# Kernel optimization log

Measured on AMD Instinct MI355X. Metric: run time of the kernel, lower is better.

Reference implementation:

```python
import jax, jax.numpy as jnp
import numpy as np
import math

S, B, L, D = 4096, 2048, 256, 128  # substructure pool, batch, max substructs/drug, hidden


def setup_inputs() -> dict:
    key = jax.random.key(0)
    ks = jax.random.split(key, 6)
    sub_feat = jax.random.normal(ks[0], (S, D), dtype=jnp.float32)
    sub_index = jax.random.randint(ks[1], (B, L), 0, S)
    # ragged lengths -> padded prefix mask (1.0 = valid substructure)
    lengths = jax.random.randint(ks[2], (B,), 8, L + 1)
    mask = (jnp.arange(L)[None, :] < lengths[:, None]).astype(jnp.float32)
    scale = 1.0 / math.sqrt(D)
    Wq = jax.random.normal(ks[3], (D, D), dtype=jnp.float32) * scale
    Wk = jax.random.normal(ks[4], (D, D), dtype=jnp.float32) * scale
    bq = jnp.zeros((D,), dtype=jnp.float32)
    bk = jnp.zeros((D,), dtype=jnp.float32)
    return {"sub_feat": sub_feat, "mask": mask, "Wq": Wq, "bq": bq,
            "Wk": Wk, "bk": bk, "sub_index": sub_index}


def reference(sub_feat, mask, Wq, bq, Wk, bk, sub_index):
    # per-drug gather of substructure ('expert') features: [B, L, D]
    gathered = sub_feat[sub_index]
    # single-head Q/K projections (V is computed but unused in the original)
    q = gathered @ Wq + bq  # [B, L, D]
    k = gathered @ Wk + bk  # [B, L, D]
    inv_sqrt_d = 1.0 / math.sqrt(D)
    # additive mask: (1 - m) * -10000 broadcast over query dim
    add_mask = (1.0 - mask)[:, None, :] * -10000.0  # [B, 1, L]
    scores = jnp.einsum('bid,bjd->bij', q, k) * inv_sqrt_d + add_mask  # [B, L, L]
    probs = jax.nn.softmax(scores, axis=-1)
    # O[:, 0, 0, :] in the original: head 0, query position 0
    score = probs[:, 0, :]  # [B, L]
    # drug_feat[i] = score[i] @ sub_feat[sub_index[i]]
    drug_embeddings = jnp.einsum('bl,bld->bd', score, gathered)  # [B, D]
    return drug_embeddings
```

## Files before the change

### kernel.cpp

```cpp
#include <hip/hip_runtime.h>

#define DIM 128
#define LEN 256
#define INV_SQRT_D 0.08838834764831845f
#define LOG2E 1.4426950408889634f
#define SCALE_L2 (INV_SQRT_D * LOG2E)

#define WS_MT   0
#define WS_C    (DIM * DIM)
#define WS_W2   (DIM * DIM + DIM)
#define WS_BQBK (DIM * DIM + 2 * DIM)
#define WS_BF   (DIM * DIM + 2 * DIM + 8)

__device__ __forceinline__ float bl(unsigned u) { return __uint_as_float(u << 16); }
__device__ __forceinline__ float bh(unsigned u) { return __uint_as_float(u & 0xffff0000u); }

__global__ __launch_bounds__(256) void prep_kernel(
    const float* __restrict__ sub_feat,
    const float* __restrict__ Wq, const float* __restrict__ bq,
    const float* __restrict__ Wk, const float* __restrict__ bk,
    float* __restrict__ ws, ushort* __restrict__ bfb, int n4)
{
    const int t   = threadIdx.x;
    const int bid = blockIdx.x;

    if (bid < DIM) {
        if (t < DIM) {
            __shared__ float wqj[DIM];
            wqj[t] = Wq[bid * DIM + t];
            __syncthreads();
            const float4* row = reinterpret_cast<const float4*>(Wk + t * DIM);
            float acc = 0.f;
            #pragma unroll 8
            for (int i = 0; i < DIM / 4; ++i) {
                float4 u = row[i];
                acc = fmaf(u.x, wqj[4*i+0], acc);
                acc = fmaf(u.y, wqj[4*i+1], acc);
                acc = fmaf(u.z, wqj[4*i+2], acc);
                acc = fmaf(u.w, wqj[4*i+3], acc);
            }
            ws[WS_MT + bid * DIM + t] = acc;
        } else {
            __syncthreads();
        }
    } else if (bid == DIM) {
        if (t < DIM) {
            __shared__ float bqs[DIM], bks[DIM], red[DIM];
            bqs[t] = bq[t]; bks[t] = bk[t];
            __syncthreads();
            const float4* rk = reinterpret_cast<const float4*>(Wk + t * DIM);
            const float4* rq = reinterpret_cast<const float4*>(Wq + t * DIM);
            float accC = 0.f, accW = 0.f;
            #pragma unroll 8
            for (int i = 0; i < DIM / 4; ++i) {
                float4 a  = rk[i];
                float4 b2 = rq[i];
                accC = fmaf(a.x,  bqs[4*i+0], accC);
                accC = fmaf(a.y,  bqs[4*i+1], accC);
                accC = fmaf(a.z,  bqs[4*i+2], accC);
                accC = fmaf(a.w,  bqs[4*i+3], accC);
                accW = fmaf(b2.x, bks[4*i+0], accW);
                accW = fmaf(b2.y, bks[4*i+1], accW);
                accW = fmaf(b2.z, bks[4*i+2], accW);
                accW = fmaf(b2.w, bks[4*i+3], accW);
            }
            ws[WS_C  + t] = accC;
            ws[WS_W2 + t] = accW;
            red[t] = bqs[t] * bks[t];
            __syncthreads();
            if (t == 0) {
                float s = 0.f;
                for (int i = 0; i < DIM; ++i) s += red[i];
                ws[WS_BQBK] = s;
            }
        } else {
            __syncthreads(); __syncthreads();
        }
    } else {
        const int i = (bid - DIM - 1) * 256 + t;
        if (i < n4) {
            const float4 u = reinterpret_cast<const float4*>(sub_feat)[i];
            ushort4 o;
            unsigned a;
            a = __float_as_uint(u.x); o.x = (ushort)((a + 0x7fffu + ((a >> 16) & 1u)) >> 16);
            a = __float_as_uint(u.y); o.y = (ushort)((a + 0x7fffu + ((a >> 16) & 1u)) >> 16);
            a = __float_as_uint(u.z); o.z = (ushort)((a + 0x7fffu + ((a >> 16) & 1u)) >> 16);
            a = __float_as_uint(u.w); o.w = (ushort)((a + 0x7fffu + ((a >> 16) & 1u)) >> 16);
            reinterpret_cast<ushort4*>(bfb)[i] = o;
        }
    }
}

__global__ __launch_bounds__(256, 8) void main_kernel(
    const float* __restrict__ sub_feat, const ushort* __restrict__ gfeat,
    const float* __restrict__ mask, const int* __restrict__ sub_index,
    const float* __restrict__ ws, float* __restrict__ out)
{
    const int t    = threadIdx.x;
    const int lane = t & 63;
    const int wv   = t >> 6;
    const int b    = blockIdx.x;
    const int g    = lane >> 4;
    const int m16  = lane & 15;

    __shared__ float2 ibw[LEN];
    __shared__ float  g0L[DIM];
    __shared__ float  vh [2][DIM];
    __shared__ float  vL [DIM];
    __shared__ float  OW [4][DIM];
    __shared__ float  Zw [4];
    __shared__ float  qbkL;

    {
        const int   ij = sub_index[(size_t)b * LEN + t];
        const float mk = mask[(size_t)b * LEN + t];
        ibw[t] = make_float2(__int_as_float(ij), (1.f - mk) * (-10000.f * LOG2E));
    }
    if (t < 64) {
        const int r0 = sub_index[(size_t)b * LEN];
        const float2 g0p = reinterpret_cast<const float2*>(sub_feat + (size_t)r0 * DIM)[t];
        g0L[2 * t]     = g0p.x;
        g0L[2 * t + 1] = g0p.y;
        const float* w2 = ws + WS_W2;
        float qp = g0p.x * w2[2 * t] + g0p.y * w2[2 * t + 1];
        #pragma unroll
        for (int o = 32; o > 0; o >>= 1) qp += __shfl_xor(qp, o);
        if (t == 0) qbkL = (qp + ws[WS_BQBK]) * SCALE_L2;
    }
    __syncthreads();

    {
        const int i  = t & (DIM - 1);
        const int hh = t >> 7;
        const float* Mrow = ws + WS_MT + hh * 64 * DIM;
        const float* gL   = g0L + hh * 64;
        float a = 0.f;
        #pragma unroll 8
        for (int j = 0; j < 64; ++j)
            a = fmaf(gL[j], Mrow[j * DIM + i], a);
        vh[hh][i] = a;
    }
    __syncthreads();
    if (t < DIM) {
        vL[t] = (vh[0][t] + vh[1][t] + ws[WS_C + t]) * SCALE_L2;
    }
    __syncthreads();

    const float4 va = reinterpret_cast<const float4*>(vL)[2 * m16];
    const float4 vb = reinterpret_cast<const float4*>(vL)[2 * m16 + 1];
    const float qterm = qbkL;

    float Zr = 0.f;
    float O0=0.f,O1=0.f,O2=0.f,O3=0.f,O4=0.f,O5=0.f,O6=0.f,O7=0.f;

    const int jbase = wv * 64;
    #pragma unroll 4
    for (int k = 0; k < 16; ++k) {
        const float2 ibp = ibw[jbase + 4 * k + g];
        const int   ij = __float_as_int(ibp.x);
        const float bj = ibp.y;
        const uint4 u = *reinterpret_cast<const uint4*>(gfeat + (size_t)ij * DIM + 8 * m16);
        const float f0 = bl(u.x), f1 = bh(u.x), f2 = bl(u.y), f3 = bh(u.y);
        const float f4 = bl(u.z), f5 = bh(u.z), f6 = bl(u.w), f7 = bh(u.w);
        float sd = f0*va.x + f1*va.y + f2*va.z + f3*va.w
                 + f4*vb.x + f5*vb.y + f6*vb.z + f7*vb.w;
        sd += __shfl_xor(sd, 1);
        sd += __shfl_xor(sd, 2);
        sd += __shfl_xor(sd, 4);
        sd += __shfl_xor(sd, 8);
        const float e = exp2f(sd + qterm + bj);
        Zr += e;
        O0 = fmaf(e, f0, O0); O1 = fmaf(e, f1, O1);
        O2 = fmaf(e, f2, O2); O3 = fmaf(e, f3, O3);
        O4 = fmaf(e, f4, O4); O5 = fmaf(e, f5, O5);
        O6 = fmaf(e, f6, O6); O7 = fmaf(e, f7, O7);
    }

    #pragma unroll
    for (int msk = 16; msk <= 32; msk <<= 1) {
        Zr += __shfl_xor(Zr, msk);
        O0 += __shfl_xor(O0, msk); O1 += __shfl_xor(O1, msk);
        O2 += __shfl_xor(O2, msk); O3 += __shfl_xor(O3, msk);
        O4 += __shfl_xor(O4, msk); O5 += __shfl_xor(O5, msk);
        O6 += __shfl_xor(O6, msk); O7 += __shfl_xor(O7, msk);
    }
    if (lane < 16) {
        reinterpret_cast<float4*>(&OW[wv][0])[2 * m16]     = make_float4(O0, O1, O2, O3);
        reinterpret_cast<float4*>(&OW[wv][0])[2 * m16 + 1] = make_float4(O4, O5, O6, O7);
    }
    if (lane == 0) Zw[wv] = Zr;
    __syncthreads();

    if (t < DIM) {
        const float Zt = Zw[0] + Zw[1] + Zw[2] + Zw[3];
        out[(size_t)b * DIM + t] =
            (OW[0][t] + OW[1][t] + OW[2][t] + OW[3][t]) / Zt;
    }
}

__global__ __launch_bounds__(256) void fused_fallback(
    const float* __restrict__ sub_feat, const float* __restrict__ mask,
    const int* __restrict__ sub_index, const float* __restrict__ ws,
    float* __restrict__ out)
{
    const int t    = threadIdx.x;
    const int lane = t & 63;
    const int wv   = t >> 6;
    const int b    = blockIdx.x;
    const int g    = lane >> 4;
    const int m16  = lane & 15;

    __shared__ float2 ibw[LEN];
    __shared__ float  g0L[DIM];
    __shared__ float  vh [2][DIM];
    __shared__ float  vL [DIM];
    __shared__ float  OW [4][DIM];
    __shared__ float  Zw [4];
    __shared__ float  qbkL;

    {
        const int   ij = sub_index[(size_t)b * LEN + t];
        const float mk = mask[(size_t)b * LEN + t];
        ibw[t] = make_float2(__int_as_float(ij), (1.f - mk) * (-10000.f * LOG2E));
    }
    if (t < 64) {
        const int r0 = sub_index[(size_t)b * LEN];
        const float2 g0p = reinterpret_cast<const float2*>(sub_feat + (size_t)r0 * DIM)[t];
        g0L[2 * t]     = g0p.x;
        g0L[2 * t + 1] = g0p.y;
        const float* w2 = ws + WS_W2;
        float qp = g0p.x * w2[2 * t] + g0p.y * w2[2 * t + 1];
        #pragma unroll
        for (int o = 32; o > 0; o >>= 1) qp += __shfl_xor(qp, o);
        if (t == 0) qbkL = (qp + ws[WS_BQBK]) * SCALE_L2;
    }
    __syncthreads();
    {
        const int i  = t & (DIM - 1);
        const int hh = t >> 7;
        const float* Mrow = ws + WS_MT + hh * 64 * DIM;
        const float* gL   = g0L + hh * 64;
        float a = 0.f;
        #pragma unroll 8
        for (int j = 0; j < 64; ++j)
            a = fmaf(gL[j], Mrow[j * DIM + i], a);
        vh[hh][i] = a;
    }
    __syncthreads();
    if (t < DIM) vL[t] = (vh[0][t] + vh[1][t] + ws[WS_C + t]) * SCALE_L2;
    __syncthreads();

    const float4 vAa = reinterpret_cast<const float4*>(vL)[2 * m16];
    const float4 vBb = reinterpret_cast<const float4*>(vL)[2 * m16 + 1];
    const float qterm = qbkL;

    float Zr = 0.f;
    float O0=0.f,O1=0.f,O2=0.f,O3=0.f,O4=0.f,O5=0.f,O6=0.f,O7=0.f;
    const int jbase = wv * 64;
    #pragma unroll 4
    for (int k = 0; k < 16; ++k) {
        const float2 ibp = ibw[jbase + 4 * k + g];
        const int   ij = __float_as_int(ibp.x);
        const float bj = ibp.y;
        const float* rp = sub_feat + (size_t)ij * DIM + 8 * m16;
        const float4 u0 = *reinterpret_cast<const float4*>(rp);
        const float4 u1 = *reinterpret_cast<const float4*>(rp + 4);
        float sd = u0.x*vAa.x + u0.y*vAa.y + u0.z*vAa.z + u0.w*vAa.w
                 + u1.x*vBb.x + u1.y*vBb.y + u1.z*vBb.z + u1.w*vBb.w;
        sd += __shfl_xor(sd, 1);
        sd += __shfl_xor(sd, 2);
        sd += __shfl_xor(sd, 4);
        sd += __shfl_xor(sd, 8);
        const float e = exp2f(sd + qterm + bj);
        Zr += e;
        O0 = fmaf(e, u0.x, O0); O1 = fmaf(e, u0.y, O1);
        O2 = fmaf(e, u0.z, O2); O3 = fmaf(e, u0.w, O3);
        O4 = fmaf(e, u1.x, O4); O5 = fmaf(e, u1.y, O5);
        O6 = fmaf(e, u1.z, O6); O7 = fmaf(e, u1.w, O7);
    }
    #pragma unroll
    for (int msk = 16; msk <= 32; msk <<= 1) {
        Zr += __shfl_xor(Zr, msk);
        O0 += __shfl_xor(O0, msk); O1 += __shfl_xor(O1, msk);
        O2 += __shfl_xor(O2, msk); O3 += __shfl_xor(O3, msk);
        O4 += __shfl_xor(O4, msk); O5 += __shfl_xor(O5, msk);
        O6 += __shfl_xor(O6, msk); O7 += __shfl_xor(O7, msk);
    }
    if (lane < 16) {
        reinterpret_cast<float4*>(&OW[wv][0])[2 * m16]     = make_float4(O0, O1, O2, O3);
        reinterpret_cast<float4*>(&OW[wv][0])[2 * m16 + 1] = make_float4(O4, O5, O6, O7);
    }
    if (lane == 0) Zw[wv] = Zr;
    __syncthreads();

    if (t < DIM) {
        const float Zt = Zw[0] + Zw[1] + Zw[2] + Zw[3];
        out[(size_t)b * DIM + t] =
            (OW[0][t] + OW[1][t] + OW[2][t] + OW[3][t]) / Zt;
    }
}

extern "C" void kernel_launch(void* const* d_in, const int* in_sizes, int n_in,
                              void* d_out, int out_size, void* d_ws, size_t ws_size,
                              hipStream_t stream) {
    const float* sub_feat  = (const float*)d_in[0];
    const float* mask      = (const float*)d_in[1];
    const float* Wq        = (const float*)d_in[2];
    const float* bq        = (const float*)d_in[3];
    const float* Wk        = (const float*)d_in[4];
    const float* bk        = (const float*)d_in[5];
    const int*   sub_index = (const int*)d_in[6];
    float* outp = (float*)d_out;
    float* ws   = (float*)d_ws;

    const int B  = in_sizes[6] / LEN;
    const int SD = in_sizes[0];
    const int n4 = SD / 4;

    const size_t needed = ((size_t)WS_BF + (size_t)(SD + 1) / 2) * sizeof(float);

    if (ws_size >= needed) {
        ushort* bfb = reinterpret_cast<ushort*>(ws + WS_BF);
        const int cvt_blocks = (n4 + 255) / 256;
        prep_kernel<<<dim3(DIM + 1 + cvt_blocks), dim3(256), 0, stream>>>(
            sub_feat, Wq, bq, Wk, bk, ws, bfb, n4);
        main_kernel<<<dim3(B), dim3(256), 0, stream>>>(
            sub_feat, bfb, mask, sub_index, ws, outp);
    } else {
        prep_kernel<<<dim3(DIM + 1), dim3(256), 0, stream>>>(
            sub_feat, Wq, bq, Wk, bk, ws, nullptr, 0);
        fused_fallback<<<dim3(B), dim3(256), 0, stream>>>(
            sub_feat, mask, sub_index, ws, outp);
    }
}
```

Before: 29.32 us.

## Fuse prep and main kernels into one cooperative launch with grid sync

Merges the weight-folding/bf16-conversion prep kernel and the per-drug attention kernel into a single cooperative kernel. Prep blocks do their prep work, every block stages its indices and mask, and a grid-wide sync separates the phases. The aim is to remove the second kernel launch and the gap between the two kernels. In exchange it adds a grid barrier and host-side device-property and occupancy queries on every call, and it only takes this path when all B blocks can be resident at once.

```diff
diff --git a/kernel.cpp b/kernel.cpp
--- a/kernel.cpp
+++ b/kernel.cpp
@@ -1,4 +1,7 @@
 #include <hip/hip_runtime.h>
+#include <hip/hip_cooperative_groups.h>
+
+namespace cg = cooperative_groups;
 
 #define DIM 128
 #define LEN 256
@@ -15,20 +18,27 @@
 __device__ __forceinline__ float bl(unsigned u) { return __uint_as_float(u << 16); }
 __device__ __forceinline__ float bh(unsigned u) { return __uint_as_float(u & 0xffff0000u); }
 
-__global__ __launch_bounds__(256) void prep_kernel(
+struct MainSmem {
+    float2 ibw[LEN];
+    float  g0L[DIM];
+    float  vh[2][DIM];
+    float  vL[DIM];
+    float  OW[4][DIM];
+    float  Zw[4];
+    float  qbkL;
+};
+
+__device__ __forceinline__ void prep_unit(int unit, int t,
     const float* __restrict__ sub_feat,
     const float* __restrict__ Wq, const float* __restrict__ bq,
     const float* __restrict__ Wk, const float* __restrict__ bk,
     float* __restrict__ ws, ushort* __restrict__ bfb, int n4)
 {
-    const int t   = threadIdx.x;
-    const int bid = blockIdx.x;
-
-    if (bid < DIM) {
+    if (unit < DIM) {
+        __shared__ float wqj[DIM];
+        if (t < DIM) wqj[t] = Wq[unit * DIM + t];
+        __syncthreads();
         if (t < DIM) {
-            __shared__ float wqj[DIM];
-            wqj[t] = Wq[bid * DIM + t];
-            __syncthreads();
             const float4* row = reinterpret_cast<const float4*>(Wk + t * DIM);
             float acc = 0.f;
             #pragma unroll 8
@@ -39,15 +49,13 @@
                 acc = fmaf(u.z, wqj[4*i+2], acc);
                 acc = fmaf(u.w, wqj[4*i+3], acc);
             }
-            ws[WS_MT + bid * DIM + t] = acc;
-        } else {
-            __syncthreads();
-        }
-    } else if (bid == DIM) {
+            ws[WS_MT + unit * DIM + t] = acc;
+        }
+    } else if (unit == DIM) {
+        __shared__ float bqs[DIM], bks[DIM], red[DIM];
+        if (t < DIM) { bqs[t] = bq[t]; bks[t] = bk[t]; }
+        __syncthreads();
         if (t < DIM) {
-            __shared__ float bqs[DIM], bks[DIM], red[DIM];
-            bqs[t] = bq[t]; bks[t] = bk[t];
-            __syncthreads();
             const float4* rk = reinterpret_cast<const float4*>(Wk + t * DIM);
             const float4* rq = reinterpret_cast<const float4*>(Wq + t * DIM);
             float accC = 0.f, accW = 0.f;
@@ -67,17 +75,15 @@
             ws[WS_C  + t] = accC;
             ws[WS_W2 + t] = accW;
             red[t] = bqs[t] * bks[t];
-            __syncthreads();
-            if (t == 0) {
-                float s = 0.f;
-                for (int i = 0; i < DIM; ++i) s += red[i];
-                ws[WS_BQBK] = s;
-            }
-        } else {
-            __syncthreads(); __syncthreads();
+        }
+        __syncthreads();
+        if (t == 0) {
+            float s = 0.f;
+            for (int i = 0; i < DIM; ++i) s += red[i];
+            ws[WS_BQBK] = s;
         }
     } else {
-        const int i = (bid - DIM - 1) * 256 + t;
+        const int i = (unit - DIM - 1) * 256 + t;
         if (i < n4) {
             const float4 u = reinterpret_cast<const float4*>(sub_feat)[i];
             ushort4 o;
@@ -91,64 +97,56 @@
     }
 }
 
-__global__ __launch_bounds__(256, 8) void main_kernel(
-    const float* __restrict__ sub_feat, const ushort* __restrict__ gfeat,
-    const float* __restrict__ mask, const int* __restrict__ sub_index,
-    const float* __restrict__ ws, float* __restrict__ out)
-{
-    const int t    = threadIdx.x;
-    const int lane = t & 63;
-    const int wv   = t >> 6;
-    const int b    = blockIdx.x;
-    const int g    = lane >> 4;
-    const int m16  = lane & 15;
-
-    __shared__ float2 ibw[LEN];
-    __shared__ float  g0L[DIM];
-    __shared__ float  vh [2][DIM];
-    __shared__ float  vL [DIM];
-    __shared__ float  OW [4][DIM];
-    __shared__ float  Zw [4];
-    __shared__ float  qbkL;
-
-    {
-        const int   ij = sub_index[(size_t)b * LEN + t];
-        const float mk = mask[(size_t)b * LEN + t];
-        ibw[t] = make_float2(__int_as_float(ij), (1.f - mk) * (-10000.f * LOG2E));
-    }
+__device__ __forceinline__ void stage_unit(int b, int t, MainSmem& sm,
+    const float* __restrict__ sub_feat, const float* __restrict__ mask,
+    const int* __restrict__ sub_index)
+{
+    const int   ij = sub_index[(size_t)b * LEN + t];
+    const float mk = mask[(size_t)b * LEN + t];
+    sm.ibw[t] = make_float2(__int_as_float(ij), (1.f - mk) * (-10000.f * LOG2E));
     if (t < 64) {
         const int r0 = sub_index[(size_t)b * LEN];
         const float2 g0p = reinterpret_cast<const float2*>(sub_feat + (size_t)r0 * DIM)[t];
-        g0L[2 * t]     = g0p.x;
-        g0L[2 * t + 1] = g0p.y;
+        sm.g0L[2 * t]     = g0p.x;
+        sm.g0L[2 * t + 1] = g0p.y;
+    }
+}
+
+template<bool BF16>
+__device__ __forceinline__ void main_rest(int b, int t, MainSmem& sm,
+    const float* __restrict__ sub_feat, const ushort* __restrict__ gfeat,
+    const float* __restrict__ ws, float* __restrict__ out)
+{
+    const int lane = t & 63;
+    const int wv   = t >> 6;
+    const int g    = lane >> 4;
+    const int m16  = lane & 15;
+
+    if (t < 64) {
         const float* w2 = ws + WS_W2;
-        float qp = g0p.x * w2[2 * t] + g0p.y * w2[2 * t + 1];
+        float qp = sm.g0L[2 * t] * w2[2 * t] + sm.g0L[2 * t + 1] * w2[2 * t + 1];
         #pragma unroll
         for (int o = 32; o > 0; o >>= 1) qp += __shfl_xor(qp, o);
-        if (t == 0) qbkL = (qp + ws[WS_BQBK]) * SCALE_L2;
-    }
-    __syncthreads();
-
+        if (t == 0) sm.qbkL = (qp + ws[WS_BQBK]) * SCALE_L2;
+    }
     {
         const int i  = t & (DIM - 1);
         const int hh = t >> 7;
         const float* Mrow = ws + WS_MT + hh * 64 * DIM;
-        const float* gL   = g0L + hh * 64;
+        const float* gL   = sm.g0L + hh * 64;
         float a = 0.f;
         #pragma unroll 8
         for (int j = 0; j < 64; ++j)
             a = fmaf(gL[j], Mrow[j * DIM + i], a);
-        vh[hh][i] = a;
-    }
-    __syncthreads();
-    if (t < DIM) {
-        vL[t] = (vh[0][t] + vh[1][t] + ws[WS_C + t]) * SCALE_L2;
-    }
-    __syncthreads();
-
-    const float4 va = reinterpret_cast<const float4*>(vL)[2 * m16];
-    const float4 vb = reinterpret_cast<const float4*>(vL)[2 * m16 + 1];
-    const float qterm = qbkL;
+        sm.vh[hh][i] = a;
+    }
+    __syncthreads();
+    if (t < DIM) sm.vL[t] = (sm.vh[0][t] + sm.vh[1][t] + ws[WS_C + t]) * SCALE_L2;
+    __syncthreads();
+
+    const float4 va = reinterpret_cast<const float4*>(sm.vL)[2 * m16];
+    const float4 vb = reinterpret_cast<const float4*>(sm.vL)[2 * m16 + 1];
+    const float qterm = sm.qbkL;
 
     float Zr = 0.f;
     float O0=0.f,O1=0.f,O2=0.f,O3=0.f,O4=0.f,O5=0.f,O6=0.f,O7=0.f;
@@ -156,12 +154,21 @@
     const int jbase = wv * 64;
     #pragma unroll 4
     for (int k = 0; k < 16; ++k) {
-        const float2 ibp = ibw[jbase + 4 * k + g];
+        const float2 ibp = sm.ibw[jbase + 4 * k + g];
         const int   ij = __float_as_int(ibp.x);
         const float bj = ibp.y;
-        const uint4 u = *reinterpret_cast<const uint4*>(gfeat + (size_t)ij * DIM + 8 * m16);
-        const float f0 = bl(u.x), f1 = bh(u.x), f2 = bl(u.y), f3 = bh(u.y);
-        const float f4 = bl(u.z), f5 = bh(u.z), f6 = bl(u.w), f7 = bh(u.w);
+        float f0, f1, f2, f3, f4, f5, f6, f7;
+        if constexpr (BF16) {
+            const uint4 u = *reinterpret_cast<const uint4*>(gfeat + (size_t)ij * DIM + 8 * m16);
+            f0 = bl(u.x); f1 = bh(u.x); f2 = bl(u.y); f3 = bh(u.y);
+            f4 = bl(u.z); f5 = bh(u.z); f6 = bl(u.w); f7 = bh(u.w);
+        } else {
+            const float* rp = sub_feat + (size_t)ij * DIM + 8 * m16;
+            const float4 u0 = *reinterpret_cast<const float4*>(rp);
+            const float4 u1 = *reinterpret_cast<const float4*>(rp + 4);
+            f0 = u0.x; f1 = u0.y; f2 = u0.z; f3 = u0.w;
+            f4 = u1.x; f5 = u1.y; f6 = u1.z; f7 = u1.w;
+        }
         float sd = f0*va.x + f1*va.y + f2*va.z + f3*va.w
                  + f4*vb.x + f5*vb.y + f6*vb.z + f7*vb.w;
         sd += __shfl_xor(sd, 1);
@@ -185,119 +192,68 @@
         O6 += __shfl_xor(O6, msk); O7 += __shfl_xor(O7, msk);
     }
     if (lane < 16) {
-        reinterpret_cast<float4*>(&OW[wv][0])[2 * m16]     = make_float4(O0, O1, O2, O3);
-        reinterpret_cast<float4*>(&OW[wv][0])[2 * m16 + 1] = make_float4(O4, O5, O6, O7);
-    }
-    if (lane == 0) Zw[wv] = Zr;
+        reinterpret_cast<float4*>(&sm.OW[wv][0])[2 * m16]     = make_float4(O0, O1, O2, O3);
+        reinterpret_cast<float4*>(&sm.OW[wv][0])[2 * m16 + 1] = make_float4(O4, O5, O6, O7);
+    }
+    if (lane == 0) sm.Zw[wv] = Zr;
     __syncthreads();
 
     if (t < DIM) {
-        const float Zt = Zw[0] + Zw[1] + Zw[2] + Zw[3];
+        const float Zt = sm.Zw[0] + sm.Zw[1] + sm.Zw[2] + sm.Zw[3];
         out[(size_t)b * DIM + t] =
-            (OW[0][t] + OW[1][t] + OW[2][t] + OW[3][t]) / Zt;
-    }
-}
-
-__global__ __launch_bounds__(256) void fused_fallback(
+            (sm.OW[0][t] + sm.OW[1][t] + sm.OW[2][t] + sm.OW[3][t]) / Zt;
+    }
+}
+
+__global__ __launch_bounds__(256, 8) void coop_kernel(
     const float* __restrict__ sub_feat, const float* __restrict__ mask,
-    const int* __restrict__ sub_index, const float* __restrict__ ws,
-    float* __restrict__ out)
-{
-    const int t    = threadIdx.x;
-    const int lane = t & 63;
-    const int wv   = t >> 6;
-    const int b    = blockIdx.x;
-    const int g    = lane >> 4;
-    const int m16  = lane & 15;
-
-    __shared__ float2 ibw[LEN];
-    __shared__ float  g0L[DIM];
-    __shared__ float  vh [2][DIM];
-    __shared__ float  vL [DIM];
-    __shared__ float  OW [4][DIM];
-    __shared__ float  Zw [4];
-    __shared__ float  qbkL;
-
-    {
-        const int   ij = sub_index[(size_t)b * LEN + t];
-        const float mk = mask[(size_t)b * LEN + t];
-        ibw[t] = make_float2(__int_as_float(ij), (1.f - mk) * (-10000.f * LOG2E));
-    }
-    if (t < 64) {
-        const int r0 = sub_index[(size_t)b * LEN];
-        const float2 g0p = reinterpret_cast<const float2*>(sub_feat + (size_t)r0 * DIM)[t];
-        g0L[2 * t]     = g0p.x;
-        g0L[2 * t + 1] = g0p.y;
-        const float* w2 = ws + WS_W2;
-        float qp = g0p.x * w2[2 * t] + g0p.y * w2[2 * t + 1];
-        #pragma unroll
-        for (int o = 32; o > 0; o >>= 1) qp += __shfl_xor(qp, o);
-        if (t == 0) qbkL = (qp + ws[WS_BQBK]) * SCALE_L2;
-    }
-    __syncthreads();
-    {
-        const int i  = t & (DIM - 1);
-        const int hh = t >> 7;
-        const float* Mrow = ws + WS_MT + hh * 64 * DIM;
-        const float* gL   = g0L + hh * 64;
-        float a = 0.f;
-        #pragma unroll 8
-        for (int j = 0; j < 64; ++j)
-            a = fmaf(gL[j], Mrow[j * DIM + i], a);
-        vh[hh][i] = a;
-    }
-    __syncthreads();
-    if (t < DIM) vL[t] = (vh[0][t] + vh[1][t] + ws[WS_C + t]) * SCALE_L2;
-    __syncthreads();
-
-    const float4 vAa = reinterpret_cast<const float4*>(vL)[2 * m16];
-    const float4 vBb = reinterpret_cast<const float4*>(vL)[2 * m16 + 1];
-    const float qterm = qbkL;
-
-    float Zr = 0.f;
-    float O0=0.f,O1=0.f,O2=0.f,O3=0.f,O4=0.f,O5=0.f,O6=0.f,O7=0.f;
-    const int jbase = wv * 64;
-    #pragma unroll 4
-    for (int k = 0; k < 16; ++k) {
-        const float2 ibp = ibw[jbase + 4 * k + g];
-        const int   ij = __float_as_int(ibp.x);
-        const float bj = ibp.y;
-        const float* rp = sub_feat + (size_t)ij * DIM + 8 * m16;
-        const float4 u0 = *reinterpret_cast<const float4*>(rp);
-        const float4 u1 = *reinterpret_cast<const float4*>(rp + 4);
-        float sd = u0.x*vAa.x + u0.y*vAa.y + u0.z*vAa.z + u0.w*vAa.w
-                 + u1.x*vBb.x + u1.y*vBb.y + u1.z*vBb.z + u1.w*vBb.w;
-        sd += __shfl_xor(sd, 1);
-        sd += __shfl_xor(sd, 2);
-        sd += __shfl_xor(sd, 4);
-        sd += __shfl_xor(sd, 8);
-        const float e = exp2f(sd + qterm + bj);
-        Zr += e;
-        O0 = fmaf(e, u0.x, O0); O1 = fmaf(e, u0.y, O1);
-        O2 = fmaf(e, u0.z, O2); O3 = fmaf(e, u0.w, O3);
-        O4 = fmaf(e, u1.x, O4); O5 = fmaf(e, u1.y, O5);
-        O6 = fmaf(e, u1.z, O6); O7 = fmaf(e, u1.w, O7);
-    }
-    #pragma unroll
-    for (int msk = 16; msk <= 32; msk <<= 1) {
-        Zr += __shfl_xor(Zr, msk);
-        O0 += __shfl_xor(O0, msk); O1 += __shfl_xor(O1, msk);
-        O2 += __shfl_xor(O2, msk); O3 += __shfl_xor(O3, msk);
-        O4 += __shfl_xor(O4, msk); O5 += __shfl_xor(O5, msk);
-        O6 += __shfl_xor(O6, msk); O7 += __shfl_xor(O7, msk);
-    }
-    if (lane < 16) {
-        reinterpret_cast<float4*>(&OW[wv][0])[2 * m16]     = make_float4(O0, O1, O2, O3);
-        reinterpret_cast<float4*>(&OW[wv][0])[2 * m16 + 1] = make_float4(O4, O5, O6, O7);
-    }
-    if (lane == 0) Zw[wv] = Zr;
-    __syncthreads();
-
-    if (t < DIM) {
-        const float Zt = Zw[0] + Zw[1] + Zw[2] + Zw[3];
-        out[(size_t)b * DIM + t] =
-            (OW[0][t] + OW[1][t] + OW[2][t] + OW[3][t]) / Zt;
-    }
+    const float* __restrict__ Wq, const float* __restrict__ bq,
+    const float* __restrict__ Wk, const float* __restrict__ bk,
+    const int* __restrict__ sub_index, float* __restrict__ ws,
+    ushort* __restrict__ bfb, float* __restrict__ out, int n4)
+{
+    __shared__ MainSmem sm;
+    const int t   = threadIdx.x;
+    const int bid = blockIdx.x;
+    const int nprep = DIM + 1 + (n4 + 255) / 256;
+
+    if (bid < nprep) prep_unit(bid, t, sub_feat, Wq, bq, Wk, bk, ws, bfb, n4);
+    stage_unit(bid, t, sm, sub_feat, mask, sub_index);
+    if (bid < nprep) __threadfence();
+    cg::this_grid().sync();
+
+    main_rest<true>(bid, t, sm, sub_feat, bfb, ws, out);
+}
+
+__global__ __launch_bounds__(256) void prep_kernel(
+    const float* __restrict__ sub_feat,
+    const float* __restrict__ Wq, const float* __restrict__ bq,
+    const float* __restrict__ Wk, const float* __restrict__ bk,
+    float* __restrict__ ws, ushort* __restrict__ bfb, int n4)
+{
+    prep_unit(blockIdx.x, threadIdx.x, sub_feat, Wq, bq, Wk, bk, ws, bfb, n4);
+}
+
+__global__ __launch_bounds__(256, 8) void main_kernel_bf16(
+    const float* __restrict__ sub_feat, const ushort* __restrict__ gfeat,
+    const float* __restrict__ mask, const int* __restrict__ sub_index,
+    const float* __restrict__ ws, float* __restrict__ out)
+{
+    __shared__ MainSmem sm;
+    stage_unit(blockIdx.x, threadIdx.x, sm, sub_feat, mask, sub_index);
+    __syncthreads();
+    main_rest<true>(blockIdx.x, threadIdx.x, sm, sub_feat, gfeat, ws, out);
+}
+
+__global__ __launch_bounds__(256, 8) void main_kernel_f32(
+    const float* __restrict__ sub_feat,
+    const float* __restrict__ mask, const int* __restrict__ sub_index,
+    const float* __restrict__ ws, float* __restrict__ out)
+{
+    __shared__ MainSmem sm;
+    stage_unit(blockIdx.x, threadIdx.x, sm, sub_feat, mask, sub_index);
+    __syncthreads();
+    main_rest<false>(blockIdx.x, threadIdx.x, sm, sub_feat, nullptr, ws, out);
 }
 
 extern "C" void kernel_launch(void* const* d_in, const int* in_sizes, int n_in,
@@ -315,21 +271,46 @@
 
     const int B  = in_sizes[6] / LEN;
     const int SD = in_sizes[0];
-    const int n4 = SD / 4;
+    int n4 = SD / 4;
+    const int nprep = DIM + 1 + (n4 + 255) / 256;
 
     const size_t needed = ((size_t)WS_BF + (size_t)(SD + 1) / 2) * sizeof(float);
-
-    if (ws_size >= needed) {
+    const bool have_bf = (ws_size >= needed);
+
+    bool coop = false;
+    if (have_bf && B >= nprep) {
+        int dev = 0;
+        hipGetDevice(&dev);
+        hipDeviceProp_t prop;
+        if (hipGetDeviceProperties(&prop, dev) == hipSuccess && prop.cooperativeLaunch) {
+            int maxb = 0;
+            if (hipOccupancyMaxActiveBlocksPerMultiprocessor(
+                    &maxb, reinterpret_cast<const void*>(coop_kernel), 256, 0) == hipSuccess &&
+                (size_t)maxb * (size_t)prop.multiProcessorCount >= (size_t)B) {
+                coop = true;
+            }
+        }
+    }
+
+    if (coop) {
         ushort* bfb = reinterpret_cast<ushort*>(ws + WS_BF);
-        const int cvt_blocks = (n4 + 255) / 256;
-        prep_kernel<<<dim3(DIM + 1 + cvt_blocks), dim3(256), 0, stream>>>(
+        void* kargs[] = {
+            (void*)&sub_feat, (void*)&mask, (void*)&Wq, (void*)&bq,
+            (void*)&Wk, (void*)&bk, (void*)&sub_index, (void*)&ws,
+            (void*)&bfb, (void*)&outp, (void*)&n4
+        };
+        hipLaunchCooperativeKernel(reinterpret_cast<const void*>(coop_kernel),
+                                   dim3(B), dim3(256), kargs, 0, stream);
+    } else if (have_bf) {
+        ushort* bfb = reinterpret_cast<ushort*>(ws + WS_BF);
+        prep_kernel<<<dim3(nprep), dim3(256), 0, stream>>>(
             sub_feat, Wq, bq, Wk, bk, ws, bfb, n4);
-        main_kernel<<<dim3(B), dim3(256), 0, stream>>>(
+        main_kernel_bf16<<<dim3(B), dim3(256), 0, stream>>>(
             sub_feat, bfb, mask, sub_index, ws, outp);
     } else {
         prep_kernel<<<dim3(DIM + 1), dim3(256), 0, stream>>>(
             sub_feat, Wq, bq, Wk, bk, ws, nullptr, 0);
-        fused_fallback<<<dim3(B), dim3(256), 0, stream>>>(
+        main_kernel_f32<<<dim3(B), dim3(256), 0, stream>>>(
             sub_feat, mask, sub_index, ws, outp);
     }
 }
```

Result: no change. 29.38 us (+0.2%).
